# Optimization experiments

Measured on AMD Instinct MI355X. Metric: run time of the kernel, lower is better.

## Reference

```python
import jax, jax.numpy as jnp
import numpy as np


def setup_inputs() -> dict:
    key = jax.random.key(0)
    ks = jax.random.split(key, 8)
    B, H, W, C = 4, 64, 64, 64
    Cf = C // 8
    x = jax.random.normal(ks[0], (B, H, W, C), dtype=jnp.float32)
    # 1x1 conv kernels stored as [C_in, C_out] (kernel_size=1)
    w_f = jax.random.normal(ks[1], (C, Cf), dtype=jnp.float32) * 0.05
    b_f = jax.random.normal(ks[2], (Cf,), dtype=jnp.float32) * 0.05
    w_g = jax.random.normal(ks[3], (C, Cf), dtype=jnp.float32) * 0.05
    b_g = jax.random.normal(ks[4], (Cf,), dtype=jnp.float32) * 0.05
    w_h = jax.random.normal(ks[5], (C, C), dtype=jnp.float32) * 0.05
    b_h = jax.random.normal(ks[6], (C,), dtype=jnp.float32) * 0.05
    gamma = jax.random.normal(ks[7], (1,), dtype=jnp.float32) * 0.1
    return {"x": x, "w_f": w_f, "b_f": b_f, "w_g": w_g, "b_g": b_g,
            "w_h": w_h, "b_h": b_h, "gamma": gamma}


def reference(x, w_f, b_f, w_g, b_g, w_h, b_h, gamma):
    B, H, W, C = x.shape
    N = H * W
    xf = x.reshape(B, N, C)  # 1x1 conv == per-pixel linear
    f = xf @ w_f + b_f       # [B, N, C/8]
    g = xf @ w_g + b_g       # [B, N, C/8]
    h = xf @ w_h + b_h       # [B, N, C]
    # attention_map[b, i, j] = <g_i, f_j>, softmax over last axis
    scores = jnp.einsum('bic,bjc->bij', g, f)  # [B, N, N]
    attn = jax.nn.softmax(scores, axis=-1)
    out = jnp.einsum('bij,bjc->bic', attn, h)  # [B, N, C]
    out = out.reshape(B, H, W, C)
    return gamma * out + x
```

## Files before the change

### kernel.cpp

```cpp
#include <hip/hip_runtime.h>
#include <hip/hip_bf16.h>

typedef __bf16 bf16;
typedef __bf16 bf16x8 __attribute__((ext_vector_type(8)));
typedef __bf16 bf16x4 __attribute__((ext_vector_type(4)));
typedef float floatx4 __attribute__((ext_vector_type(4)));

typedef int    aint    __attribute__((may_alias));
typedef long   along   __attribute__((may_alias));
typedef float2 afloat2 __attribute__((may_alias));

#define NPIX 4096
#define BATCH 4

__device__ inline bf16x8 zero8() {
    bf16x8 v;
    #pragma unroll
    for (int i = 0; i < 8; ++i) v[i] = (bf16)0.0f;
    return v;
}

__global__ __launch_bounds__(256) void proj_kernel(
    const float* __restrict__ x,
    const float* __restrict__ w_f, const float* __restrict__ b_f,
    const float* __restrict__ w_g, const float* __restrict__ b_g,
    const float* __restrict__ w_h, const float* __restrict__ b_h,
    bf16* __restrict__ fq, bf16* __restrict__ gq, unsigned char* __restrict__ hT)
{
    __shared__ bf16 xs[64 * 72];
    __shared__ bf16 wt[80 * 72];
    __shared__ float bs[80];
    const int tid = threadIdx.x;
    const int p0 = blockIdx.x * 64;

    {
        const float4* xg = (const float4*)(x + (long)p0 * 64);
        #pragma unroll
        for (int it = 0; it < 4; ++it) {
            int i4 = tid + it * 256;
            float4 v = xg[i4];
            int row = i4 >> 4, c4 = (i4 & 15) * 4;
            bf16x4 pk;
            pk[0] = (bf16)v.x; pk[1] = (bf16)v.y; pk[2] = (bf16)v.z; pk[3] = (bf16)v.w;
            *(bf16x4*)(&xs[row * 72 + c4]) = pk;
        }
    }
    for (int idx = tid; idx < 80 * 64; idx += 256) {
        int n = idx >> 6, c = idx & 63;
        float v = (n < 8) ? w_f[c * 8 + n]
                : (n < 16) ? w_g[c * 8 + (n - 8)]
                : w_h[c * 64 + (n - 16)];
        wt[n * 72 + c] = (bf16)v;
    }
    if (tid < 80)
        bs[tid] = (tid < 8) ? b_f[tid] : (tid < 16) ? b_g[tid - 8] : b_h[tid - 16];
    __syncthreads();

    const int wv = tid >> 6, lane = tid & 63;
    const int quad = lane >> 4, l15 = lane & 15;
    const int b = blockIdx.x >> 6;
    const int n0pix = (p0 & (NPIX - 1)) + wv * 16 + quad * 4;

    bf16x8 a0 = *(const bf16x8*)(&xs[(wv * 16 + l15) * 72 + quad * 8]);
    bf16x8 a1 = *(const bf16x8*)(&xs[(wv * 16 + l15) * 72 + 32 + quad * 8]);

    #pragma unroll
    for (int nt = 0; nt < 5; ++nt) {
        float bias = bs[nt * 16 + l15];
        floatx4 acc = {bias, bias, bias, bias};
        bf16x8 b0 = *(const bf16x8*)(&wt[(nt * 16 + l15) * 72 + quad * 8]);
        bf16x8 b1 = *(const bf16x8*)(&wt[(nt * 16 + l15) * 72 + 32 + quad * 8]);
        acc = __builtin_amdgcn_mfma_f32_16x16x32_bf16(a0, b0, acc, 0, 0, 0);
        acc = __builtin_amdgcn_mfma_f32_16x16x32_bf16(a1, b1, acc, 0, 0, 0);
        if (nt == 0) {
            #pragma unroll
            for (int r = 0; r < 4; ++r) {
                long P = (long)p0 + wv * 16 + quad * 4 + r;
                bf16 v = (bf16)acc[r];
                if (l15 < 8) fq[P * 8 + l15] = v;
                else         gq[P * 8 + (l15 - 8)] = v;
            }
        } else {
            int c = nt * 16 + l15 - 16;
            int pk = __builtin_amdgcn_cvt_pk_fp8_f32(acc[0], acc[1], 0, false);
            pk     = __builtin_amdgcn_cvt_pk_fp8_f32(acc[2], acc[3], pk, true);
            *(aint*)(hT + ((long)b * 64 + c) * NPIX + n0pix) = pk;
        }
    }
}

#define FBASE 0
#define HBASE 8192
#define PBASE 45056
#define DENBASE 54272
#define LDSTOT 54528

__global__ __launch_bounds__(256) void attn_kernel(
    const bf16* __restrict__ fq, const bf16* __restrict__ gq,
    const unsigned char* __restrict__ hT, const float* __restrict__ x,
    const float* __restrict__ gamma_p, float* __restrict__ out)
{
    __shared__ char smem[LDSTOT];
    const int tid  = threadIdx.x;
    const int wv   = tid >> 6, lane = tid & 63;
    const int quad = lane >> 4, l15 = lane & 15;
    const int grp  = wv & 1, half = wv >> 1;
    const int b    = blockIdx.x >> 7, it = blockIdx.x & 127;
    const long rowbase = (long)b * NPIX + it * 32 + grp * 16;
    const float sgamma = gamma_p[0];

    bf16x8 gfrag = zero8();
    if (lane < 16) gfrag = *(const bf16x8*)(gq + (rowbase + lane) * 8);

    const char* gPtr[10]; int ldsOff[10], ldsDlt[10], gStep[10];
    #pragma unroll
    for (int k = 0; k < 10; ++k) {
        int ch = k * 256 + tid;
        if (ch < 512) {
            int h = ch >> 8, c2 = ch & 255;
            ldsOff[k] = FBASE + h * 2 * 2048 + c2 * 8;
            ldsDlt[k] = 2048;
            gPtr[k]   = (const char*)fq + (long)(b * NPIX + h * 2048) * 16 + c2 * 8;
            gStep[k]  = 128 * 16;
        } else {
            int q = ch - 512;
            int h = q >> 10, r = q & 1023, c = r >> 4, j8 = r & 15;
            ldsOff[k] = HBASE + h * 2 * 9216 + c * 144 + j8 * 8;
            ldsDlt[k] = 9216;
            gPtr[k]   = (const char*)hT + ((long)b * 64 + c) * NPIX
                        + h * 2048 + j8 * 8;
            gStep[k]  = 128;
        }
    }

    floatx4 acc[4];
    #pragma unroll
    for (int nt = 0; nt < 4; ++nt) acc[nt] = (floatx4){0.f, 0.f, 0.f, 0.f};
    float denp = 0.f;
    char* Pw = smem + PBASE + wv * 2304;

    #pragma unroll
    for (int k = 0; k < 10; ++k) {
        *(afloat2*)(smem + ldsOff[k]) = *(const float2*)gPtr[k];
        gPtr[k] += gStep[k];
    }
    __syncthreads();

    for (int t = 0; t < 16; ++t) {
        const int buf = t & 1;
        float2 pre[10];
        if (t < 15) {
            #pragma unroll
            for (int k = 0; k < 10; ++k) {
                pre[k] = *(const float2*)gPtr[k];
                gPtr[k] += gStep[k];
            }
        }
        const char* Fb = smem + FBASE + (half * 2 + buf) * 2048;
        const char* Hb = smem + HBASE + (half * 2 + buf) * 9216;

        #pragma unroll
        for (int js = 0; js < 8; ++js) {
            bf16x8 afrag = zero8();
            if (lane < 16) afrag = *(const bf16x8*)(Fb + (js * 16 + l15) * 16);
            floatx4 s = __builtin_amdgcn_mfma_f32_16x16x32_bf16(
                afrag, gfrag, (floatx4){0.f, 0.f, 0.f, 0.f}, 0, 0, 0);
            float e0 = __expf(s[0]), e1 = __expf(s[1]);
            float e2 = __expf(s[2]), e3 = __expf(s[3]);
            denp += (e0 + e1) + (e2 + e3);
            int pk = __builtin_amdgcn_cvt_pk_fp8_f32(e0, e1, 0, false);
            pk     = __builtin_amdgcn_cvt_pk_fp8_f32(e2, e3, pk, true);
            *(aint*)(Pw + l15 * 144 + js * 16 + quad * 4) = pk;
        }
        asm volatile("" ::: "memory");
        #pragma unroll
        for (int ks = 0; ks < 4; ++ks) {
            along pfrag = *(const along*)(Pw + l15 * 144 + ks * 32 + quad * 8);
            #pragma unroll
            for (int nt = 0; nt < 4; ++nt) {
                along bfrag = *(const along*)(Hb + (nt * 16 + l15) * 144 + ks * 32 + quad * 8);
                acc[nt] = __builtin_amdgcn_mfma_f32_16x16x32_fp8_fp8(pfrag, bfrag, acc[nt], 0, 0, 0);
            }
        }
        __syncthreads();
        if (t < 15) {
            #pragma unroll
            for (int k = 0; k < 10; ++k)
                *(afloat2*)(smem + ldsOff[k] + (buf ^ 1) * ldsDlt[k]) = pre[k];
        }
        __syncthreads();
    }

    denp += __shfl_xor(denp, 16);
    denp += __shfl_xor(denp, 32);

    float* denr = (float*)(smem + DENBASE);
    float* red  = (float*)smem;
    if (lane < 16) denr[half * 32 + grp * 16 + l15] = denp;
    if (half == 0) {
        #pragma unroll
        for (int nt = 0; nt < 4; ++nt)
            #pragma unroll
            for (int r = 0; r < 4; ++r)
                red[grp * 1088 + (quad * 4 + r) * 68 + nt * 16 + l15] = acc[nt][r];
    }
    __syncthreads();
    if (half == 1) {
        float rden[4];
        #pragma unroll
        for (int r = 0; r < 4; ++r) {
            int i = grp * 16 + quad * 4 + r;
            rden[r] = 1.0f / (denr[i] + denr[32 + i]);
        }
        #pragma unroll
        for (int nt = 0; nt < 4; ++nt) {
            #pragma unroll
            for (int r = 0; r < 4; ++r) {
                float num = acc[nt][r] + red[grp * 1088 + (quad * 4 + r) * 68 + nt * 16 + l15];
                long off = (rowbase + quad * 4 + r) * 64 + nt * 16 + l15;
                out[off] = sgamma * (num * rden[r]) + x[off];
            }
        }
    }
}

extern "C" void kernel_launch(void* const* d_in, const int* in_sizes, int n_in,
                              void* d_out, int out_size, void* d_ws, size_t ws_size,
                              hipStream_t stream) {
    const float* x     = (const float*)d_in[0];
    const float* w_f   = (const float*)d_in[1];
    const float* b_f   = (const float*)d_in[2];
    const float* w_g   = (const float*)d_in[3];
    const float* b_g   = (const float*)d_in[4];
    const float* w_h   = (const float*)d_in[5];
    const float* b_h   = (const float*)d_in[6];
    const float* gamma = (const float*)d_in[7];
    float* out = (float*)d_out;

    bf16* fq = (bf16*)d_ws;
    bf16* gq = fq + 16384 * 8;
    unsigned char* hT = (unsigned char*)(gq + 16384 * 8);

    proj_kernel<<<256, 256, 0, stream>>>(x, w_f, b_f, w_g, b_g, w_h, b_h, fq, gq, hT);
    attn_kernel<<<512, 256, 0, stream>>>(fq, gq, hT, x, gamma, out);
}
```

Measured before the change: 106.2 us.

## Compute softmax denominator via MFMA with ones, use exp2 and wider loads

```diff
diff --git a/kernel.cpp b/kernel.cpp
--- a/kernel.cpp
+++ b/kernel.cpp
@@ -8,10 +8,11 @@
 
 typedef int    aint    __attribute__((may_alias));
 typedef long   along   __attribute__((may_alias));
-typedef float2 afloat2 __attribute__((may_alias));
+typedef float4 afloat4 __attribute__((may_alias));
 
 #define NPIX 4096
 #define BATCH 4
+#define LOG2E 1.4426950408889634f
 
 __device__ inline bf16x8 zero8() {
     bf16x8 v;
@@ -76,9 +77,8 @@
             #pragma unroll
             for (int r = 0; r < 4; ++r) {
                 long P = (long)p0 + wv * 16 + quad * 4 + r;
-                bf16 v = (bf16)acc[r];
-                if (l15 < 8) fq[P * 8 + l15] = v;
-                else         gq[P * 8 + (l15 - 8)] = v;
+                if (l15 < 8) fq[P * 8 + l15] = (bf16)acc[r];
+                else         gq[P * 8 + (l15 - 8)] = (bf16)(acc[r] * LOG2E);
             }
         } else {
             int c = nt * 16 + l15 - 16;
@@ -92,8 +92,7 @@
 #define FBASE 0
 #define HBASE 8192
 #define PBASE 45056
-#define DENBASE 54272
-#define LDSTOT 54528
+#define LDSTOT 53760
 
 __global__ __launch_bounds__(256) void attn_kernel(
     const bf16* __restrict__ fq, const bf16* __restrict__ gq,
@@ -112,47 +111,47 @@
     bf16x8 gfrag = zero8();
     if (lane < 16) gfrag = *(const bf16x8*)(gq + (rowbase + lane) * 8);
 
-    const char* gPtr[10]; int ldsOff[10], ldsDlt[10], gStep[10];
-    #pragma unroll
-    for (int k = 0; k < 10; ++k) {
+    const char* gPtr[5]; int ldsOff[5], ldsDlt[5], gStep[5];
+    #pragma unroll
+    for (int k = 0; k < 5; ++k) {
         int ch = k * 256 + tid;
-        if (ch < 512) {
-            int h = ch >> 8, c2 = ch & 255;
-            ldsOff[k] = FBASE + h * 2 * 2048 + c2 * 8;
+        if (ch < 256) {
+            int h = ch >> 7, c4 = ch & 127;
+            ldsOff[k] = FBASE + h * 2 * 2048 + c4 * 16;
             ldsDlt[k] = 2048;
-            gPtr[k]   = (const char*)fq + (long)(b * NPIX + h * 2048) * 16 + c2 * 8;
+            gPtr[k]   = (const char*)fq + (long)(b * NPIX + h * 2048) * 16 + c4 * 16;
             gStep[k]  = 128 * 16;
         } else {
-            int q = ch - 512;
-            int h = q >> 10, r = q & 1023, c = r >> 4, j8 = r & 15;
-            ldsOff[k] = HBASE + h * 2 * 9216 + c * 144 + j8 * 8;
+            int q = ch - 256;
+            int h = q >> 9, r = q & 511, c = r >> 3, j16 = r & 7;
+            ldsOff[k] = HBASE + h * 2 * 9216 + c * 144 + j16 * 16;
             ldsDlt[k] = 9216;
             gPtr[k]   = (const char*)hT + ((long)b * 64 + c) * NPIX
-                        + h * 2048 + j8 * 8;
+                        + h * 2048 + j16 * 16;
             gStep[k]  = 128;
         }
     }
 
-    floatx4 acc[4];
-    #pragma unroll
-    for (int nt = 0; nt < 4; ++nt) acc[nt] = (floatx4){0.f, 0.f, 0.f, 0.f};
-    float denp = 0.f;
-    char* Pw = smem + PBASE + wv * 2304;
-
-    #pragma unroll
-    for (int k = 0; k < 10; ++k) {
-        *(afloat2*)(smem + ldsOff[k]) = *(const float2*)gPtr[k];
+    floatx4 acc[5];
+    #pragma unroll
+    for (int nt = 0; nt < 5; ++nt) acc[nt] = (floatx4){0.f, 0.f, 0.f, 0.f};
+    const along ones = 0x3838383838383838L;
+    char* Pw = smem + PBASE + wv * 2176;
+
+    #pragma unroll
+    for (int k = 0; k < 5; ++k) {
+        *(afloat4*)(smem + ldsOff[k]) = *(const float4*)gPtr[k];
         gPtr[k] += gStep[k];
     }
     __syncthreads();
 
     for (int t = 0; t < 16; ++t) {
         const int buf = t & 1;
-        float2 pre[10];
+        float4 pre[5];
         if (t < 15) {
             #pragma unroll
-            for (int k = 0; k < 10; ++k) {
-                pre[k] = *(const float2*)gPtr[k];
+            for (int k = 0; k < 5; ++k) {
+                pre[k] = *(const float4*)gPtr[k];
                 gPtr[k] += gStep[k];
             }
         }
@@ -165,53 +164,51 @@
             if (lane < 16) afrag = *(const bf16x8*)(Fb + (js * 16 + l15) * 16);
             floatx4 s = __builtin_amdgcn_mfma_f32_16x16x32_bf16(
                 afrag, gfrag, (floatx4){0.f, 0.f, 0.f, 0.f}, 0, 0, 0);
-            float e0 = __expf(s[0]), e1 = __expf(s[1]);
-            float e2 = __expf(s[2]), e3 = __expf(s[3]);
-            denp += (e0 + e1) + (e2 + e3);
+            float e0 = exp2f(s[0]), e1 = exp2f(s[1]);
+            float e2 = exp2f(s[2]), e3 = exp2f(s[3]);
             int pk = __builtin_amdgcn_cvt_pk_fp8_f32(e0, e1, 0, false);
             pk     = __builtin_amdgcn_cvt_pk_fp8_f32(e2, e3, pk, true);
-            *(aint*)(Pw + l15 * 144 + js * 16 + quad * 4) = pk;
+            *(aint*)(Pw + l15 * 136 + js * 16 + quad * 4) = pk;
         }
         asm volatile("" ::: "memory");
         #pragma unroll
         for (int ks = 0; ks < 4; ++ks) {
-            along pfrag = *(const along*)(Pw + l15 * 144 + ks * 32 + quad * 8);
+            along pfrag = *(const along*)(Pw + l15 * 136 + ks * 32 + quad * 8);
             #pragma unroll
             for (int nt = 0; nt < 4; ++nt) {
                 along bfrag = *(const along*)(Hb + (nt * 16 + l15) * 144 + ks * 32 + quad * 8);
                 acc[nt] = __builtin_amdgcn_mfma_f32_16x16x32_fp8_fp8(pfrag, bfrag, acc[nt], 0, 0, 0);
             }
+            acc[4] = __builtin_amdgcn_mfma_f32_16x16x32_fp8_fp8(pfrag, ones, acc[4], 0, 0, 0);
         }
         __syncthreads();
         if (t < 15) {
             #pragma unroll
-            for (int k = 0; k < 10; ++k)
-                *(afloat2*)(smem + ldsOff[k] + (buf ^ 1) * ldsDlt[k]) = pre[k];
+            for (int k = 0; k < 5; ++k)
+                *(afloat4*)(smem + ldsOff[k] + (buf ^ 1) * ldsDlt[k]) = pre[k];
         }
         __syncthreads();
     }
 
-    denp += __shfl_xor(denp, 16);
-    denp += __shfl_xor(denp, 32);
-
-    float* denr = (float*)(smem + DENBASE);
-    float* red  = (float*)smem;
-    if (lane < 16) denr[half * 32 + grp * 16 + l15] = denp;
+    float* red = (float*)smem;
     if (half == 0) {
         #pragma unroll
         for (int nt = 0; nt < 4; ++nt)
             #pragma unroll
             for (int r = 0; r < 4; ++r)
                 red[grp * 1088 + (quad * 4 + r) * 68 + nt * 16 + l15] = acc[nt][r];
+        if (l15 == 0) {
+            #pragma unroll
+            for (int r = 0; r < 4; ++r)
+                red[grp * 1088 + (quad * 4 + r) * 68 + 64] = acc[4][r];
+        }
     }
     __syncthreads();
     if (half == 1) {
         float rden[4];
         #pragma unroll
-        for (int r = 0; r < 4; ++r) {
-            int i = grp * 16 + quad * 4 + r;
-            rden[r] = 1.0f / (denr[i] + denr[32 + i]);
-        }
+        for (int r = 0; r < 4; ++r)
+            rden[r] = 1.0f / (acc[4][r] + red[grp * 1088 + (quad * 4 + r) * 68 + 64]);
         #pragma unroll
         for (int nt = 0; nt < 4; ++nt) {
             #pragma unroll
```

After: 130.1 us. +22.5%, slower.
